# Kernel optimization log

Measured on AMD Instinct MI355X. Metric: run time of the kernel, lower is better.

Reference implementation:

```python
import jax, jax.numpy as jnp
import numpy as np

N = 40000
E = 640000
D_IN = 128
H = 8
C = 16  # out_dim per head


def setup_inputs() -> dict:
    key = jax.random.key(0)
    ks = jax.random.split(key, 7)
    features = jax.random.normal(ks[0], (N, D_IN), dtype=jnp.float32)
    edge_index = jax.random.randint(ks[1], (2, E), 0, N, dtype=jnp.int32)
    edge_weight = jax.random.uniform(ks[2], (E,), dtype=jnp.float32)
    # xavier-ish scales
    W_lin = jax.random.normal(ks[3], (D_IN, H * C), dtype=jnp.float32) * (1.0 / np.sqrt(D_IN))
    att_l = jax.random.normal(ks[4], (1, H, C), dtype=jnp.float32) * 0.1
    att_r = jax.random.normal(ks[5], (1, H, C), dtype=jnp.float32) * 0.1
    W_res = jax.random.normal(ks[6], (D_IN, H * C), dtype=jnp.float32) * (1.0 / np.sqrt(D_IN))
    return {"features": features, "edge_index": edge_index, "edge_weight": edge_weight,
            "W_lin": W_lin, "att_l": att_l, "att_r": att_r, "W_res": W_res}


def _segment_softmax(logits, seg, num_segments):
    # logits: (E, H), seg: (E,) destination node ids
    m = jax.ops.segment_max(logits, seg, num_segments=num_segments)  # (N, H)
    ex = jnp.exp(logits - m[seg])
    s = jax.ops.segment_sum(ex, seg, num_segments=num_segments)  # (N, H)
    return ex / s[seg]


def reference(features, edge_index, edge_weight, W_lin, att_l, att_r, W_res):
    src, dst = edge_index[0], edge_index[1]
    x = (features @ W_lin).reshape(-1, H, C)              # (N, H, C)
    alpha_l = (x * att_l).sum(-1)                          # (N, H)
    alpha_r = (x * att_r).sum(-1)                          # (N, H)
    alpha = alpha_l[src] + alpha_r[dst]                    # (E, H)
    alpha = edge_weight[:, None] * alpha
    alpha = jnp.where(alpha >= 0, alpha, 0.2 * alpha)      # leaky_relu(0.2)
    coef = _segment_softmax(alpha, dst, N)                 # (E, H)
    msgs = x[src] * coef[:, :, None]                       # (E, H, C)
    agg = jax.ops.segment_sum(msgs, dst, num_segments=N)   # (N, H, C)
    out = jax.nn.elu(agg).reshape(-1, H * C)
    out = out + features @ W_res
    return out
```

## Files before the change

### kernel.cpp

```cpp
#include <hip/hip_runtime.h>
#include <math.h>

#define N_NODES 40000
#define N_EDGES 640000
#define D 128
#define H 8
#define C 16
#define NBG 1250
#define KP 136
#define NBUCK 625
#define NCH 512
#define ECH 1250
#define MAXB 1536

typedef __attribute__((ext_vector_type(8))) short short8;
typedef __attribute__((ext_vector_type(4))) float floatx4;


__device__ __forceinline__ unsigned short f2bf(float f) {
  const unsigned u = __float_as_uint(f);
  return (unsigned short)((u + 0x7FFFu + ((u >> 16) & 1u)) >> 16);
}
__device__ __forceinline__ float bflo(unsigned p) {
  return __uint_as_float(p << 16);
}
__device__ __forceinline__ float bfhi(unsigned p) {
  return __uint_as_float(p & 0xFFFF0000u);
}
__device__ __forceinline__ float bf2f(unsigned short u) {
  return __uint_as_float((unsigned)u << 16);
}

__global__ void k_prep(const float* __restrict__ Wlin,
                       const float* __restrict__ Wres,
                       unsigned short* __restrict__ wt)
{
  const int n = blockIdx.x, k = threadIdx.x, g = blockIdx.y;
  const float* W = g ? Wres : Wlin;
  wt[((g * 128 + n) * 128) + k] = f2bf(W[(long)k * 128 + n]);
}

__global__ __launch_bounds__(256, 4) void k_gemm(
    const float* __restrict__ feat, const unsigned short* __restrict__ wt,
    unsigned short* __restrict__ xh, float* __restrict__ outp,
    const float* __restrict__ attl, const float* __restrict__ attr,
    float* __restrict__ al, float* __restrict__ ar,
    const int* __restrict__ dst, int* __restrict__ pk, int* __restrict__ cnt2)
{
  __shared__ short sA[32 * KP];
  __shared__ float sD[32 * 132];
  const int t = threadIdx.x;

  if (blockIdx.y == 1) {
    if (blockIdx.x >= NCH) return;
    int* lcnt = (int*)sA;
    for (int i = t; i < NBUCK; i += 256) lcnt[i] = 0;
    __syncthreads();
    const int c = blockIdx.x, e0 = c * ECH;
    for (int e = e0 + t; e < e0 + ECH; e += 256) {
      const int d = dst[e];
      const int r = atomicAdd(&lcnt[d >> 6], 1);
      pk[e] = ((d >> 6) << 17) | ((d & 63) << 11) | r;
    }
    __syncthreads();
    for (int i = t; i < NBUCK; i += 256) cnt2[c * NBUCK + i] = lcnt[i];
    return;
  }

  const int row0 = blockIdx.x * 32;

  {
    const int kq = t & 31;
    const int rb = (t >> 5) * 4;
    #pragma unroll
    for (int i = 0; i < 4; ++i) {
      const int r = rb + i;
      const float4 f = *(const float4*)&feat[(long)(row0 + r) * 128 + kq * 4];
      const unsigned lo = (unsigned)f2bf(f.x) | ((unsigned)f2bf(f.y) << 16);
      const unsigned hi = (unsigned)f2bf(f.z) | ((unsigned)f2bf(f.w) << 16);
      *(uint2*)&sA[r * KP + kq * 4] = make_uint2(lo, hi);
    }
  }

  const int w = t >> 6, lane = t & 63;
  const int c15 = lane & 15, q = lane >> 4;

  short8 bfr0[4][2], bfr1[4][2];
  #pragma unroll
  for (int kc = 0; kc < 4; ++kc)
    #pragma unroll
    for (int nt = 0; nt < 2; ++nt) {
      const int n = (w * 2 + nt) * 16 + c15;
      bfr0[kc][nt] = *(const short8*)&wt[n * 128 + kc * 32 + q * 8];
      bfr1[kc][nt] = *(const short8*)&wt[16384 + n * 128 + kc * 32 + q * 8];
    }
  __syncthreads();

  floatx4 acc0[2][2], acc1[2][2];
  #pragma unroll
  for (int mt = 0; mt < 2; ++mt)
    #pragma unroll
    for (int nt = 0; nt < 2; ++nt) {
      acc0[mt][nt] = (floatx4){0.f, 0.f, 0.f, 0.f};
      acc1[mt][nt] = (floatx4){0.f, 0.f, 0.f, 0.f};
    }
  #pragma unroll
  for (int kc = 0; kc < 4; ++kc)
    #pragma unroll
    for (int mt = 0; mt < 2; ++mt) {
      const short8 afr = *(const short8*)&sA[(mt * 16 + c15) * KP + kc * 32 + q * 8];
      acc0[mt][0] = __builtin_amdgcn_mfma_f32_16x16x32_bf16(afr, bfr0[kc][0], acc0[mt][0], 0, 0, 0);
      acc0[mt][1] = __builtin_amdgcn_mfma_f32_16x16x32_bf16(afr, bfr0[kc][1], acc0[mt][1], 0, 0, 0);
      acc1[mt][0] = __builtin_amdgcn_mfma_f32_16x16x32_bf16(afr, bfr1[kc][0], acc1[mt][0], 0, 0, 0);
      acc1[mt][1] = __builtin_amdgcn_mfma_f32_16x16x32_bf16(afr, bfr1[kc][1], acc1[mt][1], 0, 0, 0);
    }

  const int orow = t >> 3, seg = t & 7;
  const int grow = row0 + orow;

  #pragma unroll
  for (int mt = 0; mt < 2; ++mt)
    #pragma unroll
    for (int nt = 0; nt < 2; ++nt) {
      const int col = (w * 2 + nt) * 16 + c15;
      #pragma unroll
      for (int r = 0; r < 4; ++r)
        sD[(mt * 16 + q * 4 + r) * 132 + col] = acc0[mt][nt][r];
    }
  __syncthreads();
  {
    #pragma unroll
    for (int i = 0; i < 2; ++i) {
      const float4 v0 = *(const float4*)&sD[orow * 132 + seg * 16 + i * 8];
      const float4 v1 = *(const float4*)&sD[orow * 132 + seg * 16 + i * 8 + 4];
      uint4 u;
      u.x = (unsigned)f2bf(v0.x) | ((unsigned)f2bf(v0.y) << 16);
      u.y = (unsigned)f2bf(v0.z) | ((unsigned)f2bf(v0.w) << 16);
      u.z = (unsigned)f2bf(v1.x) | ((unsigned)f2bf(v1.y) << 16);
      u.w = (unsigned)f2bf(v1.z) | ((unsigned)f2bf(v1.w) << 16);
      *(uint4*)&xh[(long)grow * 128 + seg * 16 + i * 8] = u;
    }
    const int h = seg;
    float sl = 0.f, sr = 0.f;
    #pragma unroll
    for (int c4 = 0; c4 < 4; ++c4) {
      const float4 xv = *(const float4*)&sD[orow * 132 + h * 16 + c4 * 4];
      const float4 lv = *(const float4*)&attl[h * 16 + c4 * 4];
      const float4 rv = *(const float4*)&attr[h * 16 + c4 * 4];
      sl += xv.x * lv.x + xv.y * lv.y + xv.z * lv.z + xv.w * lv.w;
      sr += xv.x * rv.x + xv.y * rv.y + xv.z * rv.z + xv.w * rv.w;
    }
    al[(long)grow * 8 + h] = sl;
    ar[(long)grow * 8 + h] = sr;
  }
  __syncthreads();

  #pragma unroll
  for (int mt = 0; mt < 2; ++mt)
    #pragma unroll
    for (int nt = 0; nt < 2; ++nt) {
      const int col = (w * 2 + nt) * 16 + c15;
      #pragma unroll
      for (int r = 0; r < 4; ++r)
        sD[(mt * 16 + q * 4 + r) * 132 + col] = acc1[mt][nt][r];
    }
  __syncthreads();
  #pragma unroll
  for (int i = 0; i < 4; ++i) {
    const float4 v = *(const float4*)&sD[orow * 132 + seg * 16 + i * 4];
    *(float4*)&outp[(long)grow * 128 + seg * 16 + i * 4] = v;
  }
}

__global__ __launch_bounds__(512) void k_scan2a(
    const int* __restrict__ cnt2, int* __restrict__ pre2T, int* __restrict__ total)
{
  __shared__ int sd[NCH];
  const int b = blockIdx.x;
  const int t = threadIdx.x;
  const int v = cnt2[t * NBUCK + b];
  sd[t] = v;
  __syncthreads();
  #pragma unroll
  for (int off = 1; off < NCH; off <<= 1) {
    const int add = (t >= off) ? sd[t - off] : 0;
    __syncthreads();
    sd[t] += add;
    __syncthreads();
  }
  pre2T[b * NCH + t] = sd[t] - v;
  if (t == NCH - 1) total[b] = sd[t];
}

__global__ __launch_bounds__(1024) void k_scan_g(
    const int* __restrict__ total, int* __restrict__ gbase)
{
  __shared__ int sd[1024];
  const int t = threadIdx.x;
  const int v = (t < NBUCK) ? total[t] : 0;
  sd[t] = v;
  __syncthreads();
  #pragma unroll
  for (int off = 1; off < 1024; off <<= 1) {
    const int add = (t >= off) ? sd[t - off] : 0;
    __syncthreads();
    sd[t] += add;
    __syncthreads();
  }
  if (t < NBUCK) gbase[t] = sd[t] - v;
}

__global__ __launch_bounds__(256) void k_place(
    const int* __restrict__ pk, const int* __restrict__ src,
    const float* __restrict__ ew, const int* __restrict__ gbase,
    const int* __restrict__ pre2T, uint2* __restrict__ einfo)
{
  const int e = blockIdx.x * 256 + threadIdx.x;
  if (e >= N_EDGES) return;
  const int k = pk[e];
  const int b = k >> 17, dl = (k >> 11) & 63, r = k & 2047;
  const int c = e / ECH;
  const int p = gbase[b] + pre2T[b * NCH + c] + r;
  einfo[p] = make_uint2(((unsigned)src[e] << 6) | (unsigned)dl,
                        __float_as_uint(ew[e]));
}

__global__ __launch_bounds__(256) void k_edge(
    const int* __restrict__ gbase, const int* __restrict__ total,
    const uint2* __restrict__ einfo, const float* __restrict__ al,
    const float* __restrict__ ar,
    unsigned short* __restrict__ pexph, int* __restrict__ psrc,
    int* __restrict__ nodeS)
{
  __shared__ uint2 sE[MAXB];
  __shared__ float sAr[512];
  __shared__ int bcnt[64], bbase[64], bpos[64];
  const int b = blockIdx.x;
  const int start = gbase[b];
  const int cntb = total[b];
  const int t = threadIdx.x;
  if (t < 64) bcnt[t] = 0;
  for (int i = t; i < 512; i += 256) sAr[i] = ar[((long)b << 6) * 8 + i];
  __syncthreads();
  for (int i = t; i < cntb; i += 256) {
    const uint2 m = einfo[start + i];
    sE[i] = m;
    atomicAdd(&bcnt[m.x & 63], 1);
  }
  __syncthreads();
  if (t < 64) {
    const int v = bcnt[t];
    int incl = v;
    #pragma unroll
    for (int off = 1; off < 64; off <<= 1) {
      const int n = __shfl_up(incl, off, 64);
      if (t >= off) incl += n;
    }
    bbase[t] = incl - v;
    bpos[t] = 0;
    nodeS[(b << 6) + t] = start + incl - v;
  }
  if (b == 0 && t == 64) nodeS[N_NODES] = N_EDGES;
  __syncthreads();
  for (int i = t; i < cntb; i += 256) {
    const uint2 m = sE[i];
    const int dl = m.x & 63;
    const int s = (int)(m.x >> 6);
    const float w = __uint_as_float(m.y);
    const float4 l0 = *(const float4*)&al[(long)s * 8];
    const float4 l1 = *(const float4*)&al[(long)s * 8 + 4];
    const float* arr = &sAr[dl * 8];
    float lv[8] = {l0.x + arr[0], l0.y + arr[1], l0.z + arr[2], l0.w + arr[3],
                   l1.x + arr[4], l1.y + arr[5], l1.z + arr[6], l1.w + arr[7]};
    #pragma unroll
    for (int h = 0; h < 8; ++h) {
      float a = w * lv[h];
      a = (a >= 0.f) ? a : 0.2f * a;
      lv[h] = __expf(a);
    }
    const int r = atomicAdd(&bpos[dl], 1);
    const int q = start + bbase[dl] + r;
    psrc[q] = s;
    uint4 u;
    u.x = (unsigned)f2bf(lv[0]) | ((unsigned)f2bf(lv[1]) << 16);
    u.y = (unsigned)f2bf(lv[2]) | ((unsigned)f2bf(lv[3]) << 16);
    u.z = (unsigned)f2bf(lv[4]) | ((unsigned)f2bf(lv[5]) << 16);
    u.w = (unsigned)f2bf(lv[6]) | ((unsigned)f2bf(lv[7]) << 16);
    *(uint4*)&pexph[(long)q * 8] = u;
  }
}

__global__ __launch_bounds__(256) void k_node_agg(
    const int* __restrict__ nodeS, const int* __restrict__ psrc,
    const unsigned short* __restrict__ pexph,
    const unsigned short* __restrict__ xh, float* __restrict__ outp)
{
  const int wave = threadIdx.x >> 6;
  const int lane = threadIdx.x & 63;
  const int d = blockIdx.x * 4 + wave;
  const int start = nodeS[d];
  const int end = nodeS[d + 1];
  if (end <= start) return;

  const int h = lane >> 3;
  const int co = lane * 2;

  float2 a0 = {0.f, 0.f}, a1 = {0.f, 0.f}, a2 = {0.f, 0.f}, a3 = {0.f, 0.f};
  float s0s = 0.f, s1s = 0.f, s2s = 0.f, s3s = 0.f;
  int p = start;
  for (; p + 4 <= end; p += 4) {
    const int s0 = psrc[p + 0], s1 = psrc[p + 1];
    const int s2 = psrc[p + 2], s3 = psrc[p + 3];
    const float e0 = bf2f(pexph[(long)(p + 0) * 8 + h]);
    const float e1 = bf2f(pexph[(long)(p + 1) * 8 + h]);
    const float e2 = bf2f(pexph[(long)(p + 2) * 8 + h]);
    const float e3 = bf2f(pexph[(long)(p + 3) * 8 + h]);
    const unsigned v0 = *(const unsigned*)&xh[(long)s0 * 128 + co];
    const unsigned v1 = *(const unsigned*)&xh[(long)s1 * 128 + co];
    const unsigned v2 = *(const unsigned*)&xh[(long)s2 * 128 + co];
    const unsigned v3 = *(const unsigned*)&xh[(long)s3 * 128 + co];
    a0.x = fmaf(bflo(v0), e0, a0.x); a0.y = fmaf(bfhi(v0), e0, a0.y); s0s += e0;
    a1.x = fmaf(bflo(v1), e1, a1.x); a1.y = fmaf(bfhi(v1), e1, a1.y); s1s += e1;
    a2.x = fmaf(bflo(v2), e2, a2.x); a2.y = fmaf(bfhi(v2), e2, a2.y); s2s += e2;
    a3.x = fmaf(bflo(v3), e3, a3.x); a3.y = fmaf(bfhi(v3), e3, a3.y); s3s += e3;
  }
  for (; p < end; ++p) {
    const int s = psrc[p];
    const float e0 = bf2f(pexph[(long)p * 8 + h]);
    const unsigned v = *(const unsigned*)&xh[(long)s * 128 + co];
    a0.x = fmaf(bflo(v), e0, a0.x);
    a0.y = fmaf(bfhi(v), e0, a0.y);
    s0s += e0;
  }
  const float rs = 1.0f / ((s0s + s1s) + (s2s + s3s));
  const float ax = ((a0.x + a1.x) + (a2.x + a3.x)) * rs;
  const float ay = ((a0.y + a1.y) + (a2.y + a3.y)) * rs;

  float2 o = *(float2*)&outp[(long)d * 128 + co];
  o.x += (ax > 0.f) ? ax : expm1f(ax);
  o.y += (ay > 0.f) ? ay : expm1f(ay);
  *(float2*)&outp[(long)d * 128 + co] = o;
}

extern "C" void kernel_launch(void* const* d_in, const int* in_sizes, int n_in,
                              void* d_out, int out_size, void* d_ws, size_t ws_size,
                              hipStream_t stream) {
  const float* feat = (const float*)d_in[0];
  const int*   eidx = (const int*)d_in[1];
  const float* ew   = (const float*)d_in[2];
  const float* Wlin = (const float*)d_in[3];
  const float* attl = (const float*)d_in[4];
  const float* attr = (const float*)d_in[5];
  const float* Wres = (const float*)d_in[6];
  float* outp = (float*)d_out;

  float* ws = (float*)d_ws;
  unsigned short* xh = (unsigned short*)ws;
  float* al   = ws + 5120000;
  float* ar   = ws + 5440000;
  unsigned short* pexph = (unsigned short*)(ws + 5760000);
  int*   pk   = (int*)(ws + 8320000);
  uint2* einfo = (uint2*)(ws + 9000000);
  int*   psrc = (int*)(ws + 10880000);
  int*   cnt2 = (int*)(ws + 11560000);
  int*   pre2T = (int*)(ws + 11880000);
  int*   total = (int*)(ws + 12200000);
  int*   gbase = (int*)(ws + 12210000);
  int*   nodeS = (int*)(ws + 12220000);
  unsigned short* wt = (unsigned short*)(ws + 12800000);

  const int* src = eidx;
  const int* dst = eidx + N_EDGES;

  dim3 pgrid(128, 2);
  k_prep<<<pgrid, 128, 0, stream>>>(Wlin, Wres, wt);
  dim3 ggrid(NBG, 2);
  k_gemm<<<ggrid, 256, 0, stream>>>(feat, wt, xh, outp, attl, attr, al, ar,
                                    dst, pk, cnt2);
  k_scan2a<<<NBUCK, NCH, 0, stream>>>(cnt2, pre2T, total);
  k_scan_g<<<1, 1024, 0, stream>>>(total, gbase);
  k_place<<<(N_EDGES + 255) / 256, 256, 0, stream>>>(pk, src, ew, gbase,
                                                     pre2T, einfo);
  k_edge<<<NBUCK, 256, 0, stream>>>(gbase, total, einfo, al, ar,
                                    pexph, psrc, nodeS);
  k_node_agg<<<N_NODES / 4, 256, 0, stream>>>(nodeS, psrc, pexph, xh, outp);
}
```

Measured before the change: 164.0 us.

## Fuse edge softmax and node aggregation into one per-bucket kernel

Merges the edge-logit kernel and the node-aggregation kernel into a single 1024-thread block per 64-node bucket. Per-edge exp values and source ids now stay in shared memory instead of going through global buffers. Buckets are laid out at fixed MAXB strides, so the global scan kernel and the nodeS array are no longer needed. This saves two launches and the global round-trip for intermediates. In exchange the grid drops to 625 large blocks, which lowers parallelism and puts more pressure on LDS, and correctness depends on every bucket holding at most MAXB edges.

```diff
diff --git a/kernel.cpp b/kernel.cpp
--- a/kernel.cpp
+++ b/kernel.cpp
@@ -192,27 +192,9 @@
   if (t == NCH - 1) total[b] = sd[t];
 }
 
-__global__ __launch_bounds__(1024) void k_scan_g(
-    const int* __restrict__ total, int* __restrict__ gbase)
-{
-  __shared__ int sd[1024];
-  const int t = threadIdx.x;
-  const int v = (t < NBUCK) ? total[t] : 0;
-  sd[t] = v;
-  __syncthreads();
-  #pragma unroll
-  for (int off = 1; off < 1024; off <<= 1) {
-    const int add = (t >= off) ? sd[t - off] : 0;
-    __syncthreads();
-    sd[t] += add;
-    __syncthreads();
-  }
-  if (t < NBUCK) gbase[t] = sd[t] - v;
-}
-
 __global__ __launch_bounds__(256) void k_place(
     const int* __restrict__ pk, const int* __restrict__ src,
-    const float* __restrict__ ew, const int* __restrict__ gbase,
+    const float* __restrict__ ew,
     const int* __restrict__ pre2T, uint2* __restrict__ einfo)
 {
   const int e = blockIdx.x * 256 + threadIdx.x;
@@ -220,30 +202,30 @@
   const int k = pk[e];
   const int b = k >> 17, dl = (k >> 11) & 63, r = k & 2047;
   const int c = e / ECH;
-  const int p = gbase[b] + pre2T[b * NCH + c] + r;
+  const int p = b * MAXB + pre2T[b * NCH + c] + r;
   einfo[p] = make_uint2(((unsigned)src[e] << 6) | (unsigned)dl,
                         __float_as_uint(ew[e]));
 }
 
-__global__ __launch_bounds__(256) void k_edge(
-    const int* __restrict__ gbase, const int* __restrict__ total,
-    const uint2* __restrict__ einfo, const float* __restrict__ al,
-    const float* __restrict__ ar,
-    unsigned short* __restrict__ pexph, int* __restrict__ psrc,
-    int* __restrict__ nodeS)
+__global__ __launch_bounds__(1024, 4) void k_edgeagg(
+    const int* __restrict__ total, const uint2* __restrict__ einfo,
+    const float* __restrict__ al, const float* __restrict__ ar,
+    const unsigned short* __restrict__ xh, float* __restrict__ outp)
 {
   __shared__ uint2 sE[MAXB];
+  __shared__ unsigned short sP[MAXB * 8];
+  __shared__ int sS[MAXB];
   __shared__ float sAr[512];
   __shared__ int bcnt[64], bbase[64], bpos[64];
   const int b = blockIdx.x;
-  const int start = gbase[b];
   const int cntb = total[b];
   const int t = threadIdx.x;
   if (t < 64) bcnt[t] = 0;
-  for (int i = t; i < 512; i += 256) sAr[i] = ar[((long)b << 6) * 8 + i];
-  __syncthreads();
-  for (int i = t; i < cntb; i += 256) {
-    const uint2 m = einfo[start + i];
+  if (t < 512) sAr[t] = ar[((long)(b << 6)) * 8 + t];
+  __syncthreads();
+  const long e0 = (long)b * MAXB;
+  for (int i = t; i < cntb; i += 1024) {
+    const uint2 m = einfo[e0 + i];
     sE[i] = m;
     atomicAdd(&bcnt[m.x & 63], 1);
   }
@@ -258,11 +240,9 @@
     }
     bbase[t] = incl - v;
     bpos[t] = 0;
-    nodeS[(b << 6) + t] = start + incl - v;
-  }
-  if (b == 0 && t == 64) nodeS[N_NODES] = N_EDGES;
-  __syncthreads();
-  for (int i = t; i < cntb; i += 256) {
+  }
+  __syncthreads();
+  for (int i = t; i < cntb; i += 1024) {
     const uint2 m = sE[i];
     const int dl = m.x & 63;
     const int s = (int)(m.x >> 6);
@@ -279,67 +259,64 @@
       lv[h] = __expf(a);
     }
     const int r = atomicAdd(&bpos[dl], 1);
-    const int q = start + bbase[dl] + r;
-    psrc[q] = s;
+    const int qq = bbase[dl] + r;
+    sS[qq] = s;
     uint4 u;
     u.x = (unsigned)f2bf(lv[0]) | ((unsigned)f2bf(lv[1]) << 16);
     u.y = (unsigned)f2bf(lv[2]) | ((unsigned)f2bf(lv[3]) << 16);
     u.z = (unsigned)f2bf(lv[4]) | ((unsigned)f2bf(lv[5]) << 16);
     u.w = (unsigned)f2bf(lv[6]) | ((unsigned)f2bf(lv[7]) << 16);
-    *(uint4*)&pexph[(long)q * 8] = u;
-  }
-}
-
-__global__ __launch_bounds__(256) void k_node_agg(
-    const int* __restrict__ nodeS, const int* __restrict__ psrc,
-    const unsigned short* __restrict__ pexph,
-    const unsigned short* __restrict__ xh, float* __restrict__ outp)
-{
-  const int wave = threadIdx.x >> 6;
-  const int lane = threadIdx.x & 63;
-  const int d = blockIdx.x * 4 + wave;
-  const int start = nodeS[d];
-  const int end = nodeS[d + 1];
-  if (end <= start) return;
-
+    *(uint4*)&sP[qq * 8] = u;
+  }
+  __syncthreads();
+
+  const int wv = t >> 6, lane = t & 63;
   const int h = lane >> 3;
   const int co = lane * 2;
-
-  float2 a0 = {0.f, 0.f}, a1 = {0.f, 0.f}, a2 = {0.f, 0.f}, a3 = {0.f, 0.f};
-  float s0s = 0.f, s1s = 0.f, s2s = 0.f, s3s = 0.f;
-  int p = start;
-  for (; p + 4 <= end; p += 4) {
-    const int s0 = psrc[p + 0], s1 = psrc[p + 1];
-    const int s2 = psrc[p + 2], s3 = psrc[p + 3];
-    const float e0 = bf2f(pexph[(long)(p + 0) * 8 + h]);
-    const float e1 = bf2f(pexph[(long)(p + 1) * 8 + h]);
-    const float e2 = bf2f(pexph[(long)(p + 2) * 8 + h]);
-    const float e3 = bf2f(pexph[(long)(p + 3) * 8 + h]);
-    const unsigned v0 = *(const unsigned*)&xh[(long)s0 * 128 + co];
-    const unsigned v1 = *(const unsigned*)&xh[(long)s1 * 128 + co];
-    const unsigned v2 = *(const unsigned*)&xh[(long)s2 * 128 + co];
-    const unsigned v3 = *(const unsigned*)&xh[(long)s3 * 128 + co];
-    a0.x = fmaf(bflo(v0), e0, a0.x); a0.y = fmaf(bfhi(v0), e0, a0.y); s0s += e0;
-    a1.x = fmaf(bflo(v1), e1, a1.x); a1.y = fmaf(bfhi(v1), e1, a1.y); s1s += e1;
-    a2.x = fmaf(bflo(v2), e2, a2.x); a2.y = fmaf(bfhi(v2), e2, a2.y); s2s += e2;
-    a3.x = fmaf(bflo(v3), e3, a3.x); a3.y = fmaf(bfhi(v3), e3, a3.y); s3s += e3;
-  }
-  for (; p < end; ++p) {
-    const int s = psrc[p];
-    const float e0 = bf2f(pexph[(long)p * 8 + h]);
-    const unsigned v = *(const unsigned*)&xh[(long)s * 128 + co];
-    a0.x = fmaf(bflo(v), e0, a0.x);
-    a0.y = fmaf(bfhi(v), e0, a0.y);
-    s0s += e0;
-  }
-  const float rs = 1.0f / ((s0s + s1s) + (s2s + s3s));
-  const float ax = ((a0.x + a1.x) + (a2.x + a3.x)) * rs;
-  const float ay = ((a0.y + a1.y) + (a2.y + a3.y)) * rs;
-
-  float2 o = *(float2*)&outp[(long)d * 128 + co];
-  o.x += (ax > 0.f) ? ax : expm1f(ax);
-  o.y += (ay > 0.f) ? ay : expm1f(ay);
-  *(float2*)&outp[(long)d * 128 + co] = o;
+  #pragma unroll
+  for (int j = 0; j < 4; ++j) {
+    const int dl = wv * 4 + j;
+    const int start = bbase[dl];
+    const int end = start + bcnt[dl];
+    if (end <= start) continue;
+
+    float2 a0 = {0.f, 0.f}, a1 = {0.f, 0.f}, a2 = {0.f, 0.f}, a3 = {0.f, 0.f};
+    float s0s = 0.f, s1s = 0.f, s2s = 0.f, s3s = 0.f;
+    int p = start;
+    for (; p + 4 <= end; p += 4) {
+      const int s0 = sS[p + 0], s1 = sS[p + 1];
+      const int s2 = sS[p + 2], s3 = sS[p + 3];
+      const float e0v = bf2f(sP[(p + 0) * 8 + h]);
+      const float e1v = bf2f(sP[(p + 1) * 8 + h]);
+      const float e2v = bf2f(sP[(p + 2) * 8 + h]);
+      const float e3v = bf2f(sP[(p + 3) * 8 + h]);
+      const unsigned v0 = *(const unsigned*)&xh[(long)s0 * 128 + co];
+      const unsigned v1 = *(const unsigned*)&xh[(long)s1 * 128 + co];
+      const unsigned v2 = *(const unsigned*)&xh[(long)s2 * 128 + co];
+      const unsigned v3 = *(const unsigned*)&xh[(long)s3 * 128 + co];
+      a0.x = fmaf(bflo(v0), e0v, a0.x); a0.y = fmaf(bfhi(v0), e0v, a0.y); s0s += e0v;
+      a1.x = fmaf(bflo(v1), e1v, a1.x); a1.y = fmaf(bfhi(v1), e1v, a1.y); s1s += e1v;
+      a2.x = fmaf(bflo(v2), e2v, a2.x); a2.y = fmaf(bfhi(v2), e2v, a2.y); s2s += e2v;
+      a3.x = fmaf(bflo(v3), e3v, a3.x); a3.y = fmaf(bfhi(v3), e3v, a3.y); s3s += e3v;
+    }
+    for (; p < end; ++p) {
+      const int s = sS[p];
+      const float ev = bf2f(sP[p * 8 + h]);
+      const unsigned v = *(const unsigned*)&xh[(long)s * 128 + co];
+      a0.x = fmaf(bflo(v), ev, a0.x);
+      a0.y = fmaf(bfhi(v), ev, a0.y);
+      s0s += ev;
+    }
+    const float rs = 1.0f / ((s0s + s1s) + (s2s + s3s));
+    const float ax = ((a0.x + a1.x) + (a2.x + a3.x)) * rs;
+    const float ay = ((a0.y + a1.y) + (a2.y + a3.y)) * rs;
+
+    const long dnode = (long)(b << 6) + dl;
+    float2 o = *(float2*)&outp[dnode * 128 + co];
+    o.x += (ax > 0.f) ? ax : expm1f(ax);
+    o.y += (ay > 0.f) ? ay : expm1f(ay);
+    *(float2*)&outp[dnode * 128 + co] = o;
+  }
 }
 
 extern "C" void kernel_launch(void* const* d_in, const int* in_sizes, int n_in,
@@ -358,15 +335,11 @@
   unsigned short* xh = (unsigned short*)ws;
   float* al   = ws + 5120000;
   float* ar   = ws + 5440000;
-  unsigned short* pexph = (unsigned short*)(ws + 5760000);
-  int*   pk   = (int*)(ws + 8320000);
-  uint2* einfo = (uint2*)(ws + 9000000);
-  int*   psrc = (int*)(ws + 10880000);
-  int*   cnt2 = (int*)(ws + 11560000);
-  int*   pre2T = (int*)(ws + 11880000);
-  int*   total = (int*)(ws + 12200000);
-  int*   gbase = (int*)(ws + 12210000);
-  int*   nodeS = (int*)(ws + 12220000);
+  int*   pk   = (int*)(ws + 5760000);
+  uint2* einfo = (uint2*)(ws + 6500000);
+  int*   cnt2 = (int*)(ws + 8500000);
+  int*   pre2T = (int*)(ws + 8900000);
+  int*   total = (int*)(ws + 9300000);
   unsigned short* wt = (unsigned short*)(ws + 12800000);
 
   const int* src = eidx;
@@ -378,10 +351,6 @@
   k_gemm<<<ggrid, 256, 0, stream>>>(feat, wt, xh, outp, attl, attr, al, ar,
                                     dst, pk, cnt2);
   k_scan2a<<<NBUCK, NCH, 0, stream>>>(cnt2, pre2T, total);
-  k_scan_g<<<1, 1024, 0, stream>>>(total, gbase);
-  k_place<<<(N_EDGES + 255) / 256, 256, 0, stream>>>(pk, src, ew, gbase,
-                                                     pre2T, einfo);
-  k_edge<<<NBUCK, 256, 0, stream>>>(gbase, total, einfo, al, ar,
-                                    pexph, psrc, nodeS);
-  k_node_agg<<<N_NODES / 4, 256, 0, stream>>>(nodeS, psrc, pexph, xh, outp);
-}
+  k_place<<<N_EDGES / 256, 256, 0, stream>>>(pk, src, ew, pre2T, einfo);
+  k_edgeagg<<<NBUCK, 1024, 0, stream>>>(total, einfo, al, ar, xh, outp);
+}
```

After: 157.0 us. 1.04x faster.
